# Kernel tuning notes

Hardware: AMD Instinct MI355X
Metric: run time of the kernel (lower is better)

## Reference

```python
import jax, jax.numpy as jnp
import numpy as np

N = 100000       # nodes
E = 1600000      # edges (before self-loops)
D = 128          # input feature dim
H = 128          # hidden width (both hidden GATConv layers)
OUT = 128        # out_channel
NEG_SLOPE = 0.2  # PyG GATConv default


def setup_inputs() -> dict:
    key = jax.random.key(0)
    ks = jax.random.split(key, 16)
    x = jax.random.normal(ks[0], (N, D), dtype=jnp.float32)
    edge_index = jax.random.randint(ks[1], (2, E), 0, N, dtype=jnp.int64)

    def layer_params(k, din, dout):
        k1, k2, k3 = jax.random.split(k, 3)
        W = jax.random.normal(k1, (din, dout), dtype=jnp.float32) * (1.0 / np.sqrt(din))
        a_src = jax.random.normal(k2, (dout,), dtype=jnp.float32) * 0.1
        a_dst = jax.random.normal(k3, (dout,), dtype=jnp.float32) * 0.1
        b = jnp.zeros((dout,), dtype=jnp.float32)
        return W, a_src, a_dst, b

    W0, as0, ad0, b0 = layer_params(ks[2], D, H)
    W1, as1, ad1, b1 = layer_params(ks[3], H, H)
    W2, as2, ad2, b2 = layer_params(ks[4], H, OUT)
    return {
        "x": x, "edge_index": edge_index,
        "W0": W0, "as0": as0, "ad0": ad0, "b0": b0,
        "W1": W1, "as1": as1, "ad1": ad1, "b1": b1,
        "W2": W2, "as2": as2, "ad2": ad2, "b2": b2,
    }


def _gat_conv(x, src, dst, W, a_src, a_dst, b):
    """PyG GATConv, heads=1: gather -> edge attention softmax (per dst) -> scatter-add."""
    h = x @ W                                  # [N, C]
    alpha_s = h @ a_src                        # [N] per-source scalar
    alpha_d = h @ a_dst                        # [N] per-dest scalar
    e = jax.nn.leaky_relu(alpha_s[src] + alpha_d[dst], NEG_SLOPE)  # [Etot]
    # numerically stable softmax over edges grouped by destination node
    m = jax.ops.segment_max(e, dst, num_segments=N)
    ex = jnp.exp(e - m[dst])
    denom = jax.ops.segment_sum(ex, dst, num_segments=N)
    w = ex / denom[dst]                        # [Etot] attention coeffs
    out = jax.ops.segment_sum(h[src] * w[:, None], dst, num_segments=N)
    return out + b


def reference(x, edge_index, W0, as0, ad0, b0, W1, as1, ad1, b1, W2, as2, ad2, b2):
    # GATConv adds self-loops by default; edge_index[0]=source j, [1]=target i
    loops = jnp.arange(N, dtype=edge_index.dtype)
    src = jnp.concatenate([edge_index[0], loops])
    dst = jnp.concatenate([edge_index[1], loops])

    h = jax.nn.relu(_gat_conv(x, src, dst, W0, as0, ad0, b0))
    h = jax.nn.relu(_gat_conv(h, src, dst, W1, as1, ad1, b1))
    return _gat_conv(h, src, dst, W2, as2, ad2, b2)
```

## Files before the change

kernel.cpp:

```cpp
#include <hip/hip_runtime.h>

#define NN 100000
#define EE 1600000
#define NB 391
#define CHUNK 2048

typedef __attribute__((ext_vector_type(8))) short bf16x8;
typedef __attribute__((ext_vector_type(4))) float f32x4;

static __device__ __forceinline__ unsigned short f2bf(float f) {
  unsigned u = __float_as_uint(f);
  u += 0x7fffu + ((u >> 16) & 1u);
  return (unsigned short)(u >> 16);
}
static __device__ __forceinline__ float bf2f(unsigned short s) {
  return __uint_as_float(((unsigned)s) << 16);
}


__global__ void zero_aux(int* __restrict__ bcnt, int* __restrict__ bfill) {
  int i = blockIdx.x * 256 + threadIdx.x;
  if (i < NB * 16) { bcnt[i] = 0; bfill[i] = 0; }
}

__launch_bounds__(256)
__global__ void bucket_hist(const int* __restrict__ dst, int* __restrict__ bcnt) {
  __shared__ int hist[NB];
  int tid = threadIdx.x;
  for (int i = tid; i < NB; i += 256) hist[i] = 0;
  __syncthreads();
  int e0 = blockIdx.x * CHUNK;
  int n = min(CHUNK, EE - e0);
  for (int i = tid; i < n; i += 256) atomicAdd(&hist[dst[e0 + i] >> 8], 1);
  __syncthreads();
  for (int i = tid; i < NB; i += 256) {
    int c = hist[i];
    if (c) atomicAdd(&bcnt[i * 16], c);
  }
}

__launch_bounds__(256)
__global__ void bucket_scan(const int* __restrict__ bcnt, int* __restrict__ bOffC,
                            int* __restrict__ offsets) {
  __shared__ int wpart[4];
  __shared__ int carryS;
  int tid = threadIdx.x, lane = tid & 63, w = tid >> 6;
  if (tid == 0) carryS = 0;
  __syncthreads();
  for (int base = 0; base < NB; base += 256) {
    int i = base + tid;
    int v = (i < NB) ? bcnt[i * 16] : 0;
    int x = v;
    #pragma unroll
    for (int d = 1; d < 64; d <<= 1) { int y = __shfl_up(x, d); if (lane >= d) x += y; }
    if (lane == 63) wpart[w] = x;
    __syncthreads();
    int wbase = 0;
    #pragma unroll
    for (int k = 0; k < 3; ++k) if (k < w) wbase += wpart[k];
    int tot = wpart[0] + wpart[1] + wpart[2] + wpart[3];
    int carry = carryS;
    if (i < NB) bOffC[i] = carry + wbase + x - v;
    __syncthreads();
    if (tid == 0) carryS = carry + tot;
    __syncthreads();
  }
  if (tid == 0) offsets[NN] = EE + NN;
}

__launch_bounds__(256)
__global__ void bucket_scatter(const int* __restrict__ ei, const int* __restrict__ bOffC,
                               int* __restrict__ bfill, long long* __restrict__ pairs) {
  __shared__ int hist[NB];
  __shared__ int lofs[NB];
  __shared__ int resv[NB];
  __shared__ long long stage[CHUNK];
  __shared__ int wpart[4];
  int tid = threadIdx.x, lane = tid & 63, w = tid >> 6;
  int e0 = blockIdx.x * CHUNK;
  int n = min(CHUNK, EE - e0);
  for (int i = tid; i < NB; i += 256) hist[i] = 0;
  __syncthreads();

  int s[8], d[8], lp[8], bk[8];
  #pragma unroll
  for (int q = 0; q < 8; ++q) {
    int i = q * 256 + tid;
    if (i < n) {
      s[q] = ei[e0 + i];
      d[q] = ei[EE + e0 + i];
      bk[q] = d[q] >> 8;
      lp[q] = atomicAdd(&hist[bk[q]], 1);
    }
  }
  __syncthreads();

  int carry = 0;
  for (int base = 0; base < NB; base += 256) {
    int i = base + tid;
    int v = (i < NB) ? hist[i] : 0;
    int x = v;
    #pragma unroll
    for (int dd = 1; dd < 64; dd <<= 1) { int y = __shfl_up(x, dd); if (lane >= dd) x += y; }
    if (lane == 63) wpart[w] = x;
    __syncthreads();
    int wbase = 0;
    #pragma unroll
    for (int k = 0; k < 3; ++k) if (k < w) wbase += wpart[k];
    int tot = wpart[0] + wpart[1] + wpart[2] + wpart[3];
    if (i < NB) lofs[i] = carry + wbase + x - v;
    __syncthreads();
    carry += tot;
  }

  #pragma unroll
  for (int q = 0; q < 8; ++q) {
    int i = q * 256 + tid;
    if (i < n) stage[lofs[bk[q]] + lp[q]] = ((long long)d[q] << 32) | (unsigned)s[q];
  }
  for (int b = tid; b < NB; b += 256) {
    int c = hist[b];
    resv[b] = c ? atomicAdd(&bfill[b * 16], c) : 0;
  }
  __syncthreads();
  for (int i = tid; i < n; i += 256) {
    long long pd = stage[i];
    int dd = (int)(pd >> 32);
    int b = dd >> 8;
    pairs[(size_t)bOffC[b] + resv[b] + (i - lofs[b])] = pd;
  }
}

__launch_bounds__(256)
__global__ void build_csr(const long long* __restrict__ pairs, const int* __restrict__ bOffC,
                          const int* __restrict__ bcnt, int* __restrict__ offsets,
                          int* __restrict__ srcs) {
  __shared__ int deg[256];
  __shared__ int intra[256];
  __shared__ int fil[256];
  __shared__ int wpart[4];
  int b = blockIdx.x, tid = threadIdx.x;
  int n0 = b << 8;
  int nodes = min(256, NN - n0);
  int ecnt = bcnt[b * 16];
  size_t pbase = (size_t)bOffC[b];
  int cbase = bOffC[b] + n0;
  deg[tid] = 0; fil[tid] = 0;
  __syncthreads();
  for (int i = tid; i < ecnt; i += 256) {
    int dd = (int)(pairs[pbase + i] >> 32);
    atomicAdd(&deg[dd - n0], 1);
  }
  __syncthreads();
  int v = (tid < nodes) ? deg[tid] + 1 : 0;
  int lane = tid & 63, w = tid >> 6;
  int x = v;
  #pragma unroll
  for (int dd = 1; dd < 64; dd <<= 1) { int y = __shfl_up(x, dd); if (lane >= dd) x += y; }
  if (lane == 63) wpart[w] = x;
  __syncthreads();
  int wbase = 0;
  #pragma unroll
  for (int k = 0; k < 3; ++k) if (k < w) wbase += wpart[k];
  int excl = wbase + x - v;
  if (tid < nodes) { intra[tid] = excl; offsets[n0 + tid] = cbase + excl; }
  __syncthreads();
  for (int i = tid; i < ecnt; i += 256) {
    long long pd = pairs[pbase + i];
    int dd = (int)(pd >> 32), ss = (int)pd;
    int ln = dd - n0;
    int p = atomicAdd(&fil[ln], 1);
    srcs[cbase + intra[ln] + p] = ss;
  }
  __syncthreads();
  if (tid < nodes) srcs[cbase + intra[tid] + deg[tid]] = n0 + tid;
}


__global__ void prep_w(const float* __restrict__ W, short* __restrict__ Whi,
                       short* __restrict__ Wlo) {
  int t = blockIdx.x * 256 + threadIdx.x;
  if (t >= 2048) return;
  int lane = t & 63, ct = (t >> 6) & 7, kt = t >> 9;
  int l4 = lane & 15, grp = lane >> 4;
  int c = ct * 16 + l4;
  int k0 = kt * 32 + grp * 8;
  bf16x8 hi, lo;
  #pragma unroll
  for (int i = 0; i < 8; ++i) {
    float w = W[(k0 + i) * 128 + c];
    unsigned short h = f2bf(w);
    hi[i] = (short)h;
    lo[i] = (short)f2bf(w - bf2f(h));
  }
  size_t off = ((size_t)(kt * 8 + ct) * 64 + lane) * 8;
  *(bf16x8*)&Whi[off] = hi;
  *(bf16x8*)&Wlo[off] = lo;
}


__launch_bounds__(256, 2)
__global__ void transform_mfma(const float* __restrict__ x,
                               const short* __restrict__ Whi, const short* __restrict__ Wlo,
                               const float* __restrict__ a_src, const float* __restrict__ a_dst,
                               unsigned short* __restrict__ hb,
                               float* __restrict__ alphaS, float* __restrict__ alphaD) {
  int tid = threadIdx.x;
  int lane = tid & 63, wid = tid >> 6;
  int l4 = lane & 15, grp = lane >> 4;
  int rbase = blockIdx.x * 128 + wid * 32;

  const float* xr[2];
  #pragma unroll
  for (int rt = 0; rt < 2; ++rt) {
    int R = rbase + rt * 16 + l4;
    xr[rt] = x + (size_t)(R < NN ? R : 0) * 128;
  }

  f32x4 acc[2][8];
  #pragma unroll
  for (int rt = 0; rt < 2; ++rt)
    #pragma unroll
    for (int ct = 0; ct < 8; ++ct) acc[rt][ct] = (f32x4)(0.f);

  #pragma unroll
  for (int kt = 0; kt < 4; ++kt) {
    bf16x8 Ahi[2], Alo[2];
    #pragma unroll
    for (int rt = 0; rt < 2; ++rt) {
      const float* p = xr[rt] + kt * 32 + grp * 8;
      float4 v0 = *(const float4*)p;
      float4 v1 = *(const float4*)(p + 4);
      float f[8] = {v0.x, v0.y, v0.z, v0.w, v1.x, v1.y, v1.z, v1.w};
      #pragma unroll
      for (int i = 0; i < 8; ++i) {
        unsigned short h = f2bf(f[i]);
        Ahi[rt][i] = (short)h;
        Alo[rt][i] = (short)f2bf(f[i] - bf2f(h));
      }
    }
    #pragma unroll
    for (int ct = 0; ct < 8; ++ct) {
      size_t off = ((size_t)(kt * 8 + ct) * 64 + lane) * 8;
      bf16x8 bh = *(const bf16x8*)&Whi[off];
      bf16x8 bl = *(const bf16x8*)&Wlo[off];
      #pragma unroll
      for (int rt = 0; rt < 2; ++rt) {
        acc[rt][ct] = __builtin_amdgcn_mfma_f32_16x16x32_bf16(Ahi[rt], bh, acc[rt][ct], 0, 0, 0);
        acc[rt][ct] = __builtin_amdgcn_mfma_f32_16x16x32_bf16(Ahi[rt], bl, acc[rt][ct], 0, 0, 0);
        acc[rt][ct] = __builtin_amdgcn_mfma_f32_16x16x32_bf16(Alo[rt], bh, acc[rt][ct], 0, 0, 0);
      }
    }
  }

  float asv[8], adv[8];
  #pragma unroll
  for (int ct = 0; ct < 8; ++ct) { asv[ct] = a_src[ct * 16 + l4]; adv[ct] = a_dst[ct * 16 + l4]; }

  #pragma unroll
  for (int rt = 0; rt < 2; ++rt) {
    #pragma unroll
    for (int reg = 0; reg < 4; ++reg) {
      float ps = 0.f, pd = 0.f;
      #pragma unroll
      for (int ct = 0; ct < 8; ++ct) {
        ps = fmaf(acc[rt][ct][reg], asv[ct], ps);
        pd = fmaf(acc[rt][ct][reg], adv[ct], pd);
      }
      #pragma unroll
      for (int mdl = 1; mdl < 16; mdl <<= 1) {
        ps += __shfl_xor(ps, mdl);
        pd += __shfl_xor(pd, mdl);
      }
      int row = rbase + rt * 16 + grp * 4 + reg;
      if (l4 == 0 && row < NN) { alphaS[row] = ps; alphaD[row] = pd; }
    }
    #pragma unroll
    for (int reg = 0; reg < 4; ++reg) {
      int row = rbase + rt * 16 + grp * 4 + reg;
      if (row < NN) {
        #pragma unroll
        for (int ct = 0; ct < 8; ++ct)
          hb[(size_t)row * 128 + ct * 16 + l4] = f2bf(acc[rt][ct][reg]);
      }
    }
  }
}


template<bool RELU>
__launch_bounds__(256)
__global__ void agg_kernel(const unsigned short* __restrict__ hb,
                           const float* __restrict__ alphaS, const float* __restrict__ alphaD,
                           const int* __restrict__ offsets, const int* __restrict__ srcs,
                           const float* __restrict__ bias, float* __restrict__ out) {
  int lane = threadIdx.x & 63;
  int node = (blockIdx.x * 256 + threadIdx.x) >> 6;
  if (node >= NN) return;
  int beg = offsets[node], end = offsets[node + 1];
  float aD = alphaD[node];

  float m = -1e30f, ssum = 0.f;
  for (int j = beg + lane; j < end; j += 64) {
    int s = srcs[j];
    float e = alphaS[s] + aD;
    e = (e >= 0.f) ? e : 0.2f * e;
    if (e > m) { ssum = ssum * __expf(m - e) + 1.f; m = e; }
    else       { ssum += __expf(e - m); }
  }
  #pragma unroll
  for (int d2 = 1; d2 < 64; d2 <<= 1) {
    float mo = __shfl_xor(m, d2), so = __shfl_xor(ssum, d2);
    float mn = fmaxf(m, mo);
    ssum = ssum * __expf(m - mn) + so * __expf(mo - mn);
    m = mn;
  }
  float inv = 1.f / ssum;

  int l4 = lane & 15, grp = lane >> 4;
  float a[8];
  #pragma unroll
  for (int i = 0; i < 8; ++i) a[i] = 0.f;

  for (int j0 = beg; j0 < end; j0 += 64) {
    int j = j0 + lane;
    int cnt = min(64, end - j0);
    int s = 0; float wgt = 0.f;
    if (j < end) {
      int sv = srcs[j];
      float e = alphaS[sv] + aD;
      e = (e >= 0.f) ? e : 0.2f * e;
      wgt = __expf(e - m) * inv;
      s = sv;
    }
    for (int jj = 0; jj < cnt; jj += 4) {
      int e2 = jj + grp;
      int sv   = __shfl(s, e2);
      float wv = __shfl(wgt, e2);
      uint4 hp = *(const uint4*)&hb[(size_t)sv * 128 + l4 * 8];
      a[0] = fmaf(wv, __uint_as_float(hp.x << 16),           a[0]);
      a[1] = fmaf(wv, __uint_as_float(hp.x & 0xffff0000u),   a[1]);
      a[2] = fmaf(wv, __uint_as_float(hp.y << 16),           a[2]);
      a[3] = fmaf(wv, __uint_as_float(hp.y & 0xffff0000u),   a[3]);
      a[4] = fmaf(wv, __uint_as_float(hp.z << 16),           a[4]);
      a[5] = fmaf(wv, __uint_as_float(hp.z & 0xffff0000u),   a[5]);
      a[6] = fmaf(wv, __uint_as_float(hp.w << 16),           a[6]);
      a[7] = fmaf(wv, __uint_as_float(hp.w & 0xffff0000u),   a[7]);
    }
  }
  #pragma unroll
  for (int i = 0; i < 8; ++i) {
    a[i] += __shfl_xor(a[i], 16);
    a[i] += __shfl_xor(a[i], 32);
  }
  if (grp == 0) {
    float4 b0 = *(const float4*)&bias[l4 * 8];
    float4 b1 = *(const float4*)&bias[l4 * 8 + 4];
    float4 o0 = {a[0] + b0.x, a[1] + b0.y, a[2] + b0.z, a[3] + b0.w};
    float4 o1 = {a[4] + b1.x, a[5] + b1.y, a[6] + b1.z, a[7] + b1.w};
    if (RELU) {
      o0.x = fmaxf(o0.x, 0.f); o0.y = fmaxf(o0.y, 0.f);
      o0.z = fmaxf(o0.z, 0.f); o0.w = fmaxf(o0.w, 0.f);
      o1.x = fmaxf(o1.x, 0.f); o1.y = fmaxf(o1.y, 0.f);
      o1.z = fmaxf(o1.z, 0.f); o1.w = fmaxf(o1.w, 0.f);
    }
    *(float4*)&out[(size_t)node * 128 + l4 * 8]     = o0;
    *(float4*)&out[(size_t)node * 128 + l4 * 8 + 4] = o1;
  }
}


extern "C" void kernel_launch(void* const* d_in, const int* in_sizes, int n_in,
                              void* d_out, int out_size, void* d_ws, size_t ws_size,
                              hipStream_t stream) {
  const float* x   = (const float*)d_in[0];
  const int*   ei  = (const int*)d_in[1];
  const float* W0  = (const float*)d_in[2];
  const float* as0 = (const float*)d_in[3];
  const float* ad0 = (const float*)d_in[4];
  const float* b0  = (const float*)d_in[5];
  const float* W1  = (const float*)d_in[6];
  const float* as1 = (const float*)d_in[7];
  const float* ad1 = (const float*)d_in[8];
  const float* b1  = (const float*)d_in[9];
  const float* W2  = (const float*)d_in[10];
  const float* as2 = (const float*)d_in[11];
  const float* ad2 = (const float*)d_in[12];
  const float* b2  = (const float*)d_in[13];
  float* out = (float*)d_out;

  long long* pairs = (long long*)d_ws;
  short* Whi = (short*)(pairs + EE);
  short* Wlo = Whi + 16384;
  unsigned short* hb = (unsigned short*)(Wlo + 16384);
  float* alphaS = (float*)(hb + (size_t)NN * 128);
  float* alphaD = alphaS + NN;
  int*   offsets = (int*)(alphaD + NN);
  int*   srcs    = offsets + NN + 1;
  int*   bcnt    = srcs + EE + NN;
  int*   bfill   = bcnt + NB * 16;
  int*   bOffC   = bfill + NB * 16;

  const int cgrid = (EE + CHUNK - 1) / CHUNK;

  zero_aux<<<(NB * 16 + 255) / 256, 256, 0, stream>>>(bcnt, bfill);
  bucket_hist<<<cgrid, 256, 0, stream>>>(ei + EE, bcnt);
  bucket_scan<<<1, 256, 0, stream>>>(bcnt, bOffC, offsets);
  bucket_scatter<<<cgrid, 256, 0, stream>>>(ei, bOffC, bfill, pairs);
  build_csr<<<NB, 256, 0, stream>>>(pairs, bOffC, bcnt, offsets, srcs);

  const int tgrid = (NN + 127) / 128;
  const int agrid = (NN + 3) / 4;

  prep_w<<<8, 256, 0, stream>>>(W0, Whi, Wlo);
  transform_mfma<<<tgrid, 256, 0, stream>>>(x, Whi, Wlo, as0, ad0, hb, alphaS, alphaD);
  agg_kernel<true><<<agrid, 256, 0, stream>>>(hb, alphaS, alphaD, offsets, srcs, b0, out);

  prep_w<<<8, 256, 0, stream>>>(W1, Whi, Wlo);
  transform_mfma<<<tgrid, 256, 0, stream>>>(out, Whi, Wlo, as1, ad1, hb, alphaS, alphaD);
  agg_kernel<true><<<agrid, 256, 0, stream>>>(hb, alphaS, alphaD, offsets, srcs, b1, out);

  prep_w<<<8, 256, 0, stream>>>(W2, Whi, Wlo);
  transform_mfma<<<tgrid, 256, 0, stream>>>(out, Whi, Wlo, as2, ad2, hb, alphaS, alphaD);
  agg_kernel<false><<<agrid, 256, 0, stream>>>(hb, alphaS, alphaD, offsets, srcs, b2, out);
}
```

Baseline: 398.0 us.

## Single-pass softmax aggregation, LDS-staged coalesced h stores, batched weight prep

```diff
diff --git a/kernel.cpp b/kernel.cpp
--- a/kernel.cpp
+++ b/kernel.cpp
@@ -177,11 +177,14 @@
 }
 
 
-__global__ void prep_w(const float* __restrict__ W, short* __restrict__ Whi,
-                       short* __restrict__ Wlo) {
+__global__ void prep_w3(const float* __restrict__ Wa, const float* __restrict__ Wb,
+                        const float* __restrict__ Wc, short* __restrict__ Whi,
+                        short* __restrict__ Wlo) {
   int t = blockIdx.x * 256 + threadIdx.x;
-  if (t >= 2048) return;
-  int lane = t & 63, ct = (t >> 6) & 7, kt = t >> 9;
+  int L = t >> 11;
+  int tt = t & 2047;
+  const float* W = (L == 0) ? Wa : (L == 1) ? Wb : Wc;
+  int lane = tt & 63, ct = (tt >> 6) & 7, kt = tt >> 9;
   int l4 = lane & 15, grp = lane >> 4;
   int c = ct * 16 + l4;
   int k0 = kt * 32 + grp * 8;
@@ -193,7 +196,7 @@
     hi[i] = (short)h;
     lo[i] = (short)f2bf(w - bf2f(h));
   }
-  size_t off = ((size_t)(kt * 8 + ct) * 64 + lane) * 8;
+  size_t off = (size_t)L * 131072 + ((size_t)(kt * 8 + ct) * 64 + lane) * 8;
   *(bf16x8*)&Whi[off] = hi;
   *(bf16x8*)&Wlo[off] = lo;
 }
@@ -205,6 +208,7 @@
                                const float* __restrict__ a_src, const float* __restrict__ a_dst,
                                unsigned short* __restrict__ hb,
                                float* __restrict__ alphaS, float* __restrict__ alphaD) {
+  __shared__ unsigned short lh[4][32][132];
   int tid = threadIdx.x;
   int lane = tid & 63, wid = tid >> 6;
   int l4 = lane & 15, grp = lane >> 4;
@@ -277,12 +281,23 @@
     }
     #pragma unroll
     for (int reg = 0; reg < 4; ++reg) {
-      int row = rbase + rt * 16 + grp * 4 + reg;
-      if (row < NN) {
-        #pragma unroll
-        for (int ct = 0; ct < 8; ++ct)
-          hb[(size_t)row * 128 + ct * 16 + l4] = f2bf(acc[rt][ct][reg]);
-      }
+      int lrow = rt * 16 + grp * 4 + reg;
+      #pragma unroll
+      for (int ct = 0; ct < 8; ++ct)
+        lh[wid][lrow][ct * 16 + l4] = f2bf(acc[rt][ct][reg]);
+    }
+  }
+
+  #pragma unroll
+  for (int it = 0; it < 8; ++it) {
+    int lrow = it * 4 + (lane >> 4);
+    int chunk = lane & 15;
+    int row = rbase + lrow;
+    if (row < NN) {
+      const unsigned short* p = &lh[wid][lrow][chunk * 8];
+      uint4 v = {*(const unsigned*)&p[0] , *(const unsigned*)&p[2],
+                 *(const unsigned*)&p[4] , *(const unsigned*)&p[6]};
+      *(uint4*)&hb[(size_t)row * 128 + chunk * 8] = v;
     }
   }
 }
@@ -300,54 +315,45 @@
   int beg = offsets[node], end = offsets[node + 1];
   float aD = alphaD[node];
 
-  float m = -1e30f, ssum = 0.f;
-  for (int j = beg + lane; j < end; j += 64) {
-    int s = srcs[j];
-    float e = alphaS[s] + aD;
-    e = (e >= 0.f) ? e : 0.2f * e;
-    if (e > m) { ssum = ssum * __expf(m - e) + 1.f; m = e; }
-    else       { ssum += __expf(e - m); }
-  }
-  #pragma unroll
-  for (int d2 = 1; d2 < 64; d2 <<= 1) {
-    float mo = __shfl_xor(m, d2), so = __shfl_xor(ssum, d2);
-    float mn = fmaxf(m, mo);
-    ssum = ssum * __expf(m - mn) + so * __expf(mo - mn);
-    m = mn;
-  }
-  float inv = 1.f / ssum;
-
   int l4 = lane & 15, grp = lane >> 4;
   float a[8];
   #pragma unroll
   for (int i = 0; i < 8; ++i) a[i] = 0.f;
+  float ssum = 0.f;
 
   for (int j0 = beg; j0 < end; j0 += 64) {
     int j = j0 + lane;
     int cnt = min(64, end - j0);
-    int s = 0; float wgt = 0.f;
+    int s = 0; float t = 0.f;
     if (j < end) {
       int sv = srcs[j];
       float e = alphaS[sv] + aD;
       e = (e >= 0.f) ? e : 0.2f * e;
-      wgt = __expf(e - m) * inv;
+      t = __expf(e);
       s = sv;
     }
+    ssum += t;
     for (int jj = 0; jj < cnt; jj += 4) {
       int e2 = jj + grp;
       int sv   = __shfl(s, e2);
-      float wv = __shfl(wgt, e2);
-      uint4 hp = *(const uint4*)&hb[(size_t)sv * 128 + l4 * 8];
-      a[0] = fmaf(wv, __uint_as_float(hp.x << 16),           a[0]);
-      a[1] = fmaf(wv, __uint_as_float(hp.x & 0xffff0000u),   a[1]);
-      a[2] = fmaf(wv, __uint_as_float(hp.y << 16),           a[2]);
-      a[3] = fmaf(wv, __uint_as_float(hp.y & 0xffff0000u),   a[3]);
-      a[4] = fmaf(wv, __uint_as_float(hp.z << 16),           a[4]);
-      a[5] = fmaf(wv, __uint_as_float(hp.z & 0xffff0000u),   a[5]);
-      a[6] = fmaf(wv, __uint_as_float(hp.w << 16),           a[6]);
-      a[7] = fmaf(wv, __uint_as_float(hp.w & 0xffff0000u),   a[7]);
-    }
-  }
+      float tv = __shfl(t, e2);
+      if (tv > 0.f) {
+        uint4 hp = *(const uint4*)&hb[(size_t)sv * 128 + l4 * 8];
+        a[0] = fmaf(tv, __uint_as_float(hp.x << 16),           a[0]);
+        a[1] = fmaf(tv, __uint_as_float(hp.x & 0xffff0000u),   a[1]);
+        a[2] = fmaf(tv, __uint_as_float(hp.y << 16),           a[2]);
+        a[3] = fmaf(tv, __uint_as_float(hp.y & 0xffff0000u),   a[3]);
+        a[4] = fmaf(tv, __uint_as_float(hp.z << 16),           a[4]);
+        a[5] = fmaf(tv, __uint_as_float(hp.z & 0xffff0000u),   a[5]);
+        a[6] = fmaf(tv, __uint_as_float(hp.w << 16),           a[6]);
+        a[7] = fmaf(tv, __uint_as_float(hp.w & 0xffff0000u),   a[7]);
+      }
+    }
+  }
+  #pragma unroll
+  for (int d2 = 1; d2 < 64; d2 <<= 1) ssum += __shfl_xor(ssum, d2);
+  float inv = 1.f / ssum;
+
   #pragma unroll
   for (int i = 0; i < 8; ++i) {
     a[i] += __shfl_xor(a[i], 16);
@@ -356,8 +362,10 @@
   if (grp == 0) {
     float4 b0 = *(const float4*)&bias[l4 * 8];
     float4 b1 = *(const float4*)&bias[l4 * 8 + 4];
-    float4 o0 = {a[0] + b0.x, a[1] + b0.y, a[2] + b0.z, a[3] + b0.w};
-    float4 o1 = {a[4] + b1.x, a[5] + b1.y, a[6] + b1.z, a[7] + b1.w};
+    float4 o0 = {fmaf(a[0], inv, b0.x), fmaf(a[1], inv, b0.y),
+                 fmaf(a[2], inv, b0.z), fmaf(a[3], inv, b0.w)};
+    float4 o1 = {fmaf(a[4], inv, b1.x), fmaf(a[5], inv, b1.y),
+                 fmaf(a[6], inv, b1.z), fmaf(a[7], inv, b1.w)};
     if (RELU) {
       o0.x = fmaxf(o0.x, 0.f); o0.y = fmaxf(o0.y, 0.f);
       o0.z = fmaxf(o0.z, 0.f); o0.w = fmaxf(o0.w, 0.f);
@@ -391,8 +399,8 @@
 
   long long* pairs = (long long*)d_ws;
   short* Whi = (short*)(pairs + EE);
-  short* Wlo = Whi + 16384;
-  unsigned short* hb = (unsigned short*)(Wlo + 16384);
+  short* Wlo = Whi + 3 * 131072;
+  unsigned short* hb = (unsigned short*)(Wlo + 3 * 131072);
   float* alphaS = (float*)(hb + (size_t)NN * 128);
   float* alphaD = alphaS + NN;
   int*   offsets = (int*)(alphaD + NN);
@@ -403,6 +411,7 @@
 
   const int cgrid = (EE + CHUNK - 1) / CHUNK;
 
+  prep_w3<<<24, 256, 0, stream>>>(W0, W1, W2, Whi, Wlo);
   zero_aux<<<(NB * 16 + 255) / 256, 256, 0, stream>>>(bcnt, bfill);
   bucket_hist<<<cgrid, 256, 0, stream>>>(ei + EE, bcnt);
   bucket_scan<<<1, 256, 0, stream>>>(bcnt, bOffC, offsets);
@@ -412,15 +421,12 @@
   const int tgrid = (NN + 127) / 128;
   const int agrid = (NN + 3) / 4;
 
-  prep_w<<<8, 256, 0, stream>>>(W0, Whi, Wlo);
   transform_mfma<<<tgrid, 256, 0, stream>>>(x, Whi, Wlo, as0, ad0, hb, alphaS, alphaD);
   agg_kernel<true><<<agrid, 256, 0, stream>>>(hb, alphaS, alphaD, offsets, srcs, b0, out);
 
-  prep_w<<<8, 256, 0, stream>>>(W1, Whi, Wlo);
-  transform_mfma<<<tgrid, 256, 0, stream>>>(out, Whi, Wlo, as1, ad1, hb, alphaS, alphaD);
+  transform_mfma<<<tgrid, 256, 0, stream>>>(out, Whi + 131072, Wlo + 131072, as1, ad1, hb, alphaS, alphaD);
   agg_kernel<true><<<agrid, 256, 0, stream>>>(hb, alphaS, alphaD, offsets, srcs, b1, out);
 
-  prep_w<<<8, 256, 0, stream>>>(W2, Whi, Wlo);
-  transform_mfma<<<tgrid, 256, 0, stream>>>(out, Whi, Wlo, as2, ad2, hb, alphaS, alphaD);
+  transform_mfma<<<tgrid, 256, 0, stream>>>(out, Whi + 262144, Wlo + 262144, as2, ad2, hb, alphaS, alphaD);
   agg_kernel<false><<<agrid, 256, 0, stream>>>(hb, alphaS, alphaD, offsets, srcs, b2, out);
 }
```

New measurement: 404.0 us. No clear change (+1.5%).
